# Kernel tuning notes

Hardware: AMD Instinct MI355X
Metric: run time of the kernel (lower is better)

Reference implementation:

```python
import jax, jax.numpy as jnp
import numpy as np

T, B, D = 1024, 4, 1024
E, K = 8, 2
H = int(round(2.0 * D))   # options.transformer_dim_scale = 2.0
O = D


def setup_inputs() -> dict:
    key = jax.random.key(0)
    ks = jax.random.split(key, 8)
    s = lambda fan: 1.0 / np.sqrt(fan)
    return {
        "x": jax.random.normal(ks[0], (T, B, D), dtype=jnp.float32),
        "sequence_mask": jnp.ones((T, B, 1), dtype=jnp.float32),
        "ln_scale": jnp.ones((D,), dtype=jnp.float32),
        "ln_bias": jnp.zeros((D,), dtype=jnp.float32),
        "router_w": jax.random.normal(ks[1], (E, D), dtype=jnp.float32) * s(D),
        "w1": jax.random.normal(ks[2], (E, D, H), dtype=jnp.float32) * s(D),
        "b1": jnp.zeros((E, H), dtype=jnp.float32),
        "w2": jax.random.normal(ks[3], (E, H, O), dtype=jnp.float32) * s(H),
        "b2": jnp.zeros((E, O), dtype=jnp.float32),
    }


def _layernorm(x, scale, bias, eps=1e-5):
    mu = jnp.mean(x, axis=-1, keepdims=True)
    var = jnp.mean(jnp.square(x - mu), axis=-1, keepdims=True)
    return (x - mu) * jax.lax.rsqrt(var + eps) * scale + bias


def reference(x, sequence_mask, ln_scale, ln_bias, router_w, w1, b1, w2, b2):
    t, b, d = x.shape
    n = t * b  # total tokens
    xn = _layernorm(x, ln_scale, ln_bias)
    x_flat = xn.reshape(n, d)                                  # [N, D]

    gate_logits = x_flat @ router_w.T                          # [N, E]
    topk_logits, topk_idx = jax.lax.top_k(gate_logits, K)      # [N, K]
    gate_probs = jax.nn.softmax(topk_logits, axis=-1)          # [N, K]
    # scatter top-k probs into a dense [N, E] combine-weight matrix
    rows = jnp.arange(n)[:, None]
    weights = jnp.zeros((n, E), dtype=x.dtype).at[rows, topk_idx].add(gate_probs)

    # dense per-expert two-layer MLP (exact GELU, dropout=0 at inference)
    h = jax.nn.gelu(jnp.einsum('nd,edh->neh', x_flat, w1) + b1, approximate=False)
    y = jax.nn.gelu(jnp.einsum('neh,eho->neo', h, w2) + b2, approximate=False)
    out = jnp.einsum('neo,ne->no', y, weights).reshape(t, b, O)

    out = out * sequence_mask                                  # multiplicative masking
    return out, gate_logits
```

## Files before the change

kernel.cpp:

```cpp
#include <hip/hip_runtime.h>
#include <hip/hip_bf16.h>
#include <math.h>

#define T_DIM 1024
#define B_DIM 4
#define D_DIM 1024
#define N_TOK (T_DIM * B_DIM)
#define E_NUM 8
#define K_TOP 2
#define H_DIM 2048
#define O_DIM 1024

typedef __attribute__((ext_vector_type(8))) short bf16x8;
typedef __attribute__((ext_vector_type(4))) float f32x4;

__device__ __forceinline__ float gelu_exact(float x) {
    return 0.5f * x * (1.0f + erff(x * 0.7071067811865476f));
}

__device__ __forceinline__ unsigned short f2bf(float f) {
    union { __hip_bfloat16 h; unsigned short u; } c;
    c.h = __float2bfloat16(f);
    return c.u;
}

__device__ __forceinline__ void gload_lds16(const void* g, void* l) {
    __builtin_amdgcn_global_load_lds(
        (const __attribute__((address_space(1))) void*)g,
        (__attribute__((address_space(3))) void*)l,
        16, 0, 0);
}

__global__ __launch_bounds__(256) void ln_router_kernel(
    const float* __restrict__ x,
    const float* __restrict__ seq_mask,
    const float* __restrict__ ln_scale,
    const float* __restrict__ ln_bias,
    const float* __restrict__ router_w,
    unsigned short* __restrict__ xn,
    float* __restrict__ gate_out,
    unsigned int* __restrict__ tok_e,
    float2* __restrict__ tok_p)
{
    const int wv = threadIdx.x >> 6;
    const int ln = threadIdx.x & 63;
    const int n = blockIdx.x * 4 + wv;

    const float* xr = x + (size_t)n * D_DIM;

    float v[4][4];
    float sum = 0.f, sumsq = 0.f;
#pragma unroll
    for (int p = 0; p < 4; ++p) {
        float4 t = *(const float4*)&xr[ln * 4 + p * 256];
        v[p][0] = t.x; v[p][1] = t.y; v[p][2] = t.z; v[p][3] = t.w;
#pragma unroll
        for (int c = 0; c < 4; ++c) { sum += v[p][c]; sumsq += v[p][c] * v[p][c]; }
    }
#pragma unroll
    for (int m = 1; m < 64; m <<= 1) {
        sum   += __shfl_xor(sum, m, 64);
        sumsq += __shfl_xor(sumsq, m, 64);
    }
    const float mu = sum * (1.0f / D_DIM);
    const float var = sumsq * (1.0f / D_DIM) - mu * mu;
    const float rstd = rsqrtf(var + 1e-5f);

    float xv[4][4];
#pragma unroll
    for (int p = 0; p < 4; ++p) {
        int col = ln * 4 + p * 256;
        float4 sc = *(const float4*)&ln_scale[col];
        float4 bi = *(const float4*)&ln_bias[col];
        const float* scp = (const float*)&sc;
        const float* bip = (const float*)&bi;
        ushort4 o;
        unsigned short* op = (unsigned short*)&o;
#pragma unroll
        for (int c = 0; c < 4; ++c) {
            float t = (v[p][c] - mu) * rstd * scp[c] + bip[c];
            xv[p][c] = t;
            op[c] = f2bf(t);
        }
        *(ushort4*)&xn[(size_t)n * D_DIM + col] = o;
    }

    float dot[E_NUM];
#pragma unroll
    for (int e = 0; e < E_NUM; ++e) {
        const float* rw = router_w + (size_t)e * D_DIM;
        float a = 0.f;
#pragma unroll
        for (int p = 0; p < 4; ++p) {
            float4 t = *(const float4*)&rw[ln * 4 + p * 256];
            const float* tp = (const float*)&t;
#pragma unroll
            for (int c = 0; c < 4; ++c) a += xv[p][c] * tp[c];
        }
        dot[e] = a;
    }
#pragma unroll
    for (int e = 0; e < E_NUM; ++e)
#pragma unroll
        for (int m = 1; m < 64; m <<= 1) dot[e] += __shfl_xor(dot[e], m, 64);

    if (ln == 0) {
        float4 g0 = make_float4(dot[0], dot[1], dot[2], dot[3]);
        float4 g1 = make_float4(dot[4], dot[5], dot[6], dot[7]);
        *(float4*)&gate_out[(size_t)n * E_NUM] = g0;
        *(float4*)&gate_out[(size_t)n * E_NUM + 4] = g1;

        int i0 = 0; float l0 = dot[0];
        for (int e = 1; e < E_NUM; ++e)
            if (dot[e] > l0) { l0 = dot[e]; i0 = e; }
        int i1 = -1; float l1 = -INFINITY;
        for (int e = 0; e < E_NUM; ++e) {
            if (e == i0) continue;
            if (dot[e] > l1) { l1 = dot[e]; i1 = e; }
        }
        float z = __expf(l1 - l0);
        float p0 = 1.0f / (1.0f + z);
        float p1 = z / (1.0f + z);
        float msk = seq_mask[n];

        tok_e[n] = (unsigned)i0 | ((unsigned)i1 << 8);
        tok_p[n] = make_float2(p0 * msk, p1 * msk);
    }
}

__global__ __launch_bounds__(256) void build_lists(
    const unsigned int* __restrict__ tok_e,
    const float2* __restrict__ tok_p,
    int* __restrict__ counts,
    int* __restrict__ perm,
    int* __restrict__ hrow,
    float* __restrict__ probs)
{
    const int e = blockIdx.x;
    const int tid = threadIdx.x;
    const int wv = tid >> 6, ln = tid & 63;
    __shared__ int s_base;
    __shared__ int wave_tot[4];
    if (tid == 0) s_base = 0;
    __syncthreads();

    for (int t0 = 0; t0 < N_TOK; t0 += 256) {
        int t = t0 + tid;
        unsigned pk = tok_e[t];
        int m1 = (((pk >> 8) & 0xffu) == (unsigned)e);
        int m = (((pk & 0xffu) == (unsigned)e) | m1);
        unsigned long long bal = __ballot(m);
        int pre = __popcll(bal & ((1ull << ln) - 1ull));
        if (ln == 0) wave_tot[wv] = __popcll(bal);
        __syncthreads();
        int base = s_base;
        int wbase = 0;
#pragma unroll
        for (int w = 0; w < 4; ++w) if (w < wv) wbase += wave_tot[w];
        int total = wave_tot[0] + wave_tot[1] + wave_tot[2] + wave_tot[3];
        __syncthreads();
        if (m) {
            int pos = base + wbase + pre;
            perm[e * N_TOK + pos] = t;
            hrow[e * N_TOK + pos] = t * 2 + m1;
            float2 p = tok_p[t];
            probs[e * N_TOK + pos] = m1 ? p.y : p.x;
        }
        if (tid == 0) s_base = base + total;
        __syncthreads();
    }
    if (tid == 0) counts[e] = s_base;
}

__global__ __launch_bounds__(256) void transpose_convert(
    const float* __restrict__ src, unsigned short* __restrict__ dst,
    int K, int N)
{
    __shared__ float ts[64][65];
    const int e = blockIdx.z;
    const int n0 = blockIdx.x * 64;
    const int k0 = blockIdx.y * 64;
    const float* S = src + (size_t)e * K * N;
    unsigned short* D = dst + (size_t)e * N * K;
    const int tid = threadIdx.x;
    const int r = tid >> 4, c4 = (tid & 15) * 4;

#pragma unroll
    for (int j = 0; j < 4; ++j) {
        float4 v = *(const float4*)&S[(size_t)(k0 + r + 16 * j) * N + n0 + c4];
        ts[r + 16 * j][c4 + 0] = v.x;
        ts[r + 16 * j][c4 + 1] = v.y;
        ts[r + 16 * j][c4 + 2] = v.z;
        ts[r + 16 * j][c4 + 3] = v.w;
    }
    __syncthreads();
#pragma unroll
    for (int j = 0; j < 4; ++j) {
        int nn = r + 16 * j;
        ushort4 o;
        o.x = f2bf(ts[c4 + 0][nn]);
        o.y = f2bf(ts[c4 + 1][nn]);
        o.z = f2bf(ts[c4 + 2][nn]);
        o.w = f2bf(ts[c4 + 3][nn]);
        *(ushort4*)&D[(size_t)(n0 + nn) * K + k0 + c4] = o;
    }
}

__global__ __launch_bounds__(256) void expert_gemm1(
    const unsigned short* __restrict__ xn,
    const unsigned short* __restrict__ wt1,
    const float* __restrict__ b1,
    const int* __restrict__ counts,
    const int* __restrict__ perm,
    const int* __restrict__ hrow,
    unsigned short* __restrict__ hbuf)
{
    const int e = blockIdx.z;
    const int cnt = counts[e];
    const int m0 = blockIdx.y * 128;
    if (m0 >= cnt) return;
    const int n0 = blockIdx.x * 128;
    const int tid = threadIdx.x;
    const int wv = tid >> 6, ln = tid & 63;
    const int ml = ln & 15, q = ln >> 4;
    const int wm = (wv & 1) * 64, wn = (wv >> 1) * 64;

    __shared__ __align__(16) unsigned char As[128 * 64];
    __shared__ __align__(16) unsigned char Bs[128 * 64];
    __shared__ int s_tok[128];
    __shared__ int s_hr[128];

    if (tid < 128) {
        int m = m0 + tid;
        int ok = (m < cnt);
        s_tok[tid] = ok ? perm[e * N_TOK + m] : 0;
        s_hr[tid]  = ok ? hrow[e * N_TOK + m] : 0;
    }
    __syncthreads();

    const unsigned short* wte = wt1 + (size_t)e * H_DIM * D_DIM;
    const unsigned short* agp[2]; int alds[2];
    const unsigned short* bgp[2]; int blds[2];
#pragma unroll
    for (int j = 0; j < 2; ++j) {
        int slot = j * 256 + wv * 64 + ln;
        int r = slot >> 2, ss = slot & 3;
        int sg = ss ^ ((r >> 1) & 3);
        agp[j] = xn + (size_t)s_tok[r] * D_DIM + sg * 8;
        alds[j] = slot * 16;
        bgp[j] = wte + (size_t)(n0 + r) * D_DIM + sg * 8;
        blds[j] = slot * 16;
    }

    f32x4 acc[4][4] = {};
    const int rslot = (q ^ ((ml >> 1) & 3)) * 16;

    for (int k0 = 0; k0 < D_DIM; k0 += 32) {
        __syncthreads();
#pragma unroll
        for (int j = 0; j < 2; ++j) {
            gload_lds16(agp[j] + k0, As + alds[j]);
            gload_lds16(bgp[j] + k0, Bs + blds[j]);
        }
        __syncthreads();
        bf16x8 af[4], bfr[4];
#pragma unroll
        for (int i = 0; i < 4; ++i)
            af[i] = *(const bf16x8*)(As + (wm + i * 16 + ml) * 64 + rslot);
#pragma unroll
        for (int j = 0; j < 4; ++j)
            bfr[j] = *(const bf16x8*)(Bs + (wn + j * 16 + ml) * 64 + rslot);
#pragma unroll
        for (int i = 0; i < 4; ++i)
#pragma unroll
            for (int j = 0; j < 4; ++j)
                acc[i][j] = __builtin_amdgcn_mfma_f32_16x16x32_bf16(
                    af[i], bfr[j], acc[i][j], 0, 0, 0);
    }

    float bias[4];
#pragma unroll
    for (int j = 0; j < 4; ++j)
        bias[j] = b1[(size_t)e * H_DIM + n0 + wn + j * 16 + ml];

#pragma unroll
    for (int i = 0; i < 4; ++i) {
#pragma unroll
        for (int r = 0; r < 4; ++r) {
            int rl = wm + i * 16 + q * 4 + r;
            if (m0 + rl < cnt) {
                int hr = s_hr[rl];
                unsigned short* dst = hbuf + (size_t)hr * H_DIM + n0 + wn + ml;
#pragma unroll
                for (int j = 0; j < 4; ++j)
                    dst[j * 16] = f2bf(gelu_exact(acc[i][j][r] + bias[j]));
            }
        }
    }
}

__global__ __launch_bounds__(256) void expert_gemm2(
    const unsigned short* __restrict__ hbuf,
    const unsigned short* __restrict__ wt2,
    const float* __restrict__ b2,
    const int* __restrict__ counts,
    const int* __restrict__ perm,
    const int* __restrict__ hrow,
    const float* __restrict__ probs,
    float* __restrict__ ybuf)
{
    const int e = blockIdx.z;
    const int cnt = counts[e];
    const int m0 = blockIdx.y * 128;
    if (m0 >= cnt) return;
    const int n0 = blockIdx.x * 128;
    const int tid = threadIdx.x;
    const int wv = tid >> 6, ln = tid & 63;
    const int ml = ln & 15, q = ln >> 4;
    const int wm = (wv & 1) * 64, wn = (wv >> 1) * 64;

    __shared__ __align__(16) unsigned char As[128 * 64];
    __shared__ __align__(16) unsigned char Bs[128 * 64];
    __shared__ int s_hr[128];
    __shared__ float s_p[128];

    if (tid < 128) {
        int m = m0 + tid;
        int ok = (m < cnt);
        s_hr[tid]  = ok ? hrow[e * N_TOK + m] : 0;
        s_p[tid]   = ok ? probs[e * N_TOK + m] : 0.f;
    }
    __syncthreads();

    const unsigned short* wte = wt2 + (size_t)e * O_DIM * H_DIM;
    const unsigned short* agp[2]; int alds[2];
    const unsigned short* bgp[2]; int blds[2];
#pragma unroll
    for (int j = 0; j < 2; ++j) {
        int slot = j * 256 + wv * 64 + ln;
        int r = slot >> 2, ss = slot & 3;
        int sg = ss ^ ((r >> 1) & 3);
        agp[j] = hbuf + (size_t)s_hr[r] * H_DIM + sg * 8;
        alds[j] = slot * 16;
        bgp[j] = wte + (size_t)(n0 + r) * H_DIM + sg * 8;
        blds[j] = slot * 16;
    }

    f32x4 acc[4][4] = {};
    const int rslot = (q ^ ((ml >> 1) & 3)) * 16;

    for (int k0 = 0; k0 < H_DIM; k0 += 32) {
        __syncthreads();
#pragma unroll
        for (int j = 0; j < 2; ++j) {
            gload_lds16(agp[j] + k0, As + alds[j]);
            gload_lds16(bgp[j] + k0, Bs + blds[j]);
        }
        __syncthreads();
        bf16x8 af[4], bfr[4];
#pragma unroll
        for (int i = 0; i < 4; ++i)
            af[i] = *(const bf16x8*)(As + (wm + i * 16 + ml) * 64 + rslot);
#pragma unroll
        for (int j = 0; j < 4; ++j)
            bfr[j] = *(const bf16x8*)(Bs + (wn + j * 16 + ml) * 64 + rslot);
#pragma unroll
        for (int i = 0; i < 4; ++i)
#pragma unroll
            for (int j = 0; j < 4; ++j)
                acc[i][j] = __builtin_amdgcn_mfma_f32_16x16x32_bf16(
                    af[i], bfr[j], acc[i][j], 0, 0, 0);
    }

    float bias[4];
#pragma unroll
    for (int j = 0; j < 4; ++j)
        bias[j] = b2[(size_t)e * O_DIM + n0 + wn + j * 16 + ml];

#pragma unroll
    for (int i = 0; i < 4; ++i) {
#pragma unroll
        for (int r = 0; r < 4; ++r) {
            int rl = wm + i * 16 + q * 4 + r;
            if (m0 + rl < cnt) {
                int hr = s_hr[rl];
                float p = s_p[rl];
                float* dst = ybuf + (size_t)hr * O_DIM + n0 + wn + ml;
#pragma unroll
                for (int j = 0; j < 4; ++j)
                    dst[j * 16] = gelu_exact(acc[i][j][r] + bias[j]) * p;
            }
        }
    }
}

__global__ __launch_bounds__(256) void combine_kernel(
    const float* __restrict__ ybuf, float* __restrict__ out)
{
    const size_t i = ((size_t)blockIdx.x * 256 + threadIdx.x) * 4;
    const size_t t = i / O_DIM;
    const size_t o = i % O_DIM;
    float4 a = *(const float4*)&ybuf[(t * 2) * O_DIM + o];
    float4 b = *(const float4*)&ybuf[(t * 2 + 1) * O_DIM + o];
    float4 r = make_float4(a.x + b.x, a.y + b.y, a.z + b.z, a.w + b.w);
    *(float4*)&out[i] = r;
}

extern "C" void kernel_launch(void* const* d_in, const int* in_sizes, int n_in,
                              void* d_out, int out_size, void* d_ws, size_t ws_size,
                              hipStream_t stream) {
    const float* x        = (const float*)d_in[0];
    const float* seq_mask = (const float*)d_in[1];
    const float* ln_scale = (const float*)d_in[2];
    const float* ln_bias  = (const float*)d_in[3];
    const float* router_w = (const float*)d_in[4];
    const float* w1       = (const float*)d_in[5];
    const float* b1       = (const float*)d_in[6];
    const float* w2       = (const float*)d_in[7];
    const float* b2       = (const float*)d_in[8];

    float* out      = (float*)d_out;
    float* gate_out = out + (size_t)N_TOK * O_DIM;

    char* ws = (char*)d_ws;
    unsigned short* xn = (unsigned short*)ws;
    ws += (size_t)N_TOK * D_DIM * 2;
    unsigned short* wt = (unsigned short*)ws;
    ws += (size_t)E_NUM * H_DIM * D_DIM * 2;
    unsigned short* hbuf = (unsigned short*)ws;
    ws += (size_t)N_TOK * K_TOP * H_DIM * 2;
    float* ybuf = (float*)ws;
    ws += (size_t)N_TOK * K_TOP * O_DIM * 4;
    unsigned int* tok_e = (unsigned int*)ws; ws += (size_t)N_TOK * 4;
    float2* tok_p = (float2*)ws; ws += (size_t)N_TOK * 8;
    int* counts = (int*)ws; ws += 256;
    int* perm = (int*)ws;  ws += (size_t)E_NUM * N_TOK * 4;
    int* hrow = (int*)ws;  ws += (size_t)E_NUM * N_TOK * 4;
    float* probs = (float*)ws;

    ln_router_kernel<<<N_TOK / 4, 256, 0, stream>>>(
        x, seq_mask, ln_scale, ln_bias, router_w,
        xn, gate_out, tok_e, tok_p);

    build_lists<<<E_NUM, 256, 0, stream>>>(
        tok_e, tok_p, counts, perm, hrow, probs);

    transpose_convert<<<dim3(H_DIM / 64, D_DIM / 64, E_NUM), 256, 0, stream>>>(
        w1, wt, D_DIM, H_DIM);

    expert_gemm1<<<dim3(H_DIM / 128, N_TOK / 128, E_NUM), 256, 0, stream>>>(
        xn, wt, b1, counts, perm, hrow, hbuf);

    transpose_convert<<<dim3(O_DIM / 64, H_DIM / 64, E_NUM), 256, 0, stream>>>(
        w2, wt, H_DIM, O_DIM);

    expert_gemm2<<<dim3(O_DIM / 128, N_TOK / 128, E_NUM), 256, 0, stream>>>(
        hbuf, wt, b2, counts, perm, hrow, probs, ybuf);

    combine_kernel<<<(N_TOK * O_DIM / 4) / 256, 256, 0, stream>>>(ybuf, out);
}
```

Before: 353.8 us.

## Compact expert tile grid and double K-step per LDS stage in expert GEMMs

Replaces the per-expert 3D grid, where most blocks exit early, with a flat grid of 72 slots that are mapped to (expert, row-tile) through a prefix sum over expert counts. Each main-loop iteration now loads a 64-wide K slab with a new swizzle and runs two MFMA sub-steps, which halves the number of barrier pairs. This cuts launch and scheduling waste and synchronisation overhead, at the cost of twice the LDS per block and possibly lower occupancy. The 72-slot cap assumes the total number of tiles across experts never exceeds that bound, which holds since 8192 routed rows split into at most 64+8 tiles.

```diff
diff --git a/kernel.cpp b/kernel.cpp
--- a/kernel.cpp
+++ b/kernel.cpp
@@ -10,6 +10,7 @@
 #define K_TOP 2
 #define H_DIM 2048
 #define O_DIM 1024
+#define MAX_YSLOTS 72
 
 typedef __attribute__((ext_vector_type(8))) short bf16x8;
 typedef __attribute__((ext_vector_type(4))) float f32x4;
@@ -206,6 +207,18 @@
     }
 }
 
+__device__ __forceinline__ int slot_to_tile(const int* counts, int yslot, int* m0) {
+    int e = -1, acc = 0, m = 0;
+#pragma unroll
+    for (int ee = 0; ee < E_NUM; ++ee) {
+        int t = (counts[ee] + 127) >> 7;
+        if (e < 0 && yslot < acc + t) { e = ee; m = (yslot - acc) << 7; }
+        acc += t;
+    }
+    *m0 = m;
+    return e;
+}
+
 __global__ __launch_bounds__(256) void expert_gemm1(
     const unsigned short* __restrict__ xn,
     const unsigned short* __restrict__ wt1,
@@ -215,18 +228,18 @@
     const int* __restrict__ hrow,
     unsigned short* __restrict__ hbuf)
 {
-    const int e = blockIdx.z;
+    int m0;
+    const int e = slot_to_tile(counts, blockIdx.y, &m0);
+    if (e < 0) return;
     const int cnt = counts[e];
-    const int m0 = blockIdx.y * 128;
-    if (m0 >= cnt) return;
     const int n0 = blockIdx.x * 128;
     const int tid = threadIdx.x;
     const int wv = tid >> 6, ln = tid & 63;
     const int ml = ln & 15, q = ln >> 4;
     const int wm = (wv & 1) * 64, wn = (wv >> 1) * 64;
 
-    __shared__ __align__(16) unsigned char As[128 * 64];
-    __shared__ __align__(16) unsigned char Bs[128 * 64];
+    __shared__ __align__(16) unsigned char As[128 * 128];
+    __shared__ __align__(16) unsigned char Bs[128 * 128];
     __shared__ int s_tok[128];
     __shared__ int s_hr[128];
 
@@ -239,13 +252,13 @@
     __syncthreads();
 
     const unsigned short* wte = wt1 + (size_t)e * H_DIM * D_DIM;
-    const unsigned short* agp[2]; int alds[2];
-    const unsigned short* bgp[2]; int blds[2];
-#pragma unroll
-    for (int j = 0; j < 2; ++j) {
-        int slot = j * 256 + wv * 64 + ln;
-        int r = slot >> 2, ss = slot & 3;
-        int sg = ss ^ ((r >> 1) & 3);
+    const unsigned short* agp[4]; int alds[4];
+    const unsigned short* bgp[4]; int blds[4];
+#pragma unroll
+    for (int j = 0; j < 4; ++j) {
+        int slot = j * 256 + tid;
+        int r = slot >> 3, c = slot & 7;
+        int sg = (c & 4) | ((c & 3) ^ ((r >> 1) & 3));
         agp[j] = xn + (size_t)s_tok[r] * D_DIM + sg * 8;
         alds[j] = slot * 16;
         bgp[j] = wte + (size_t)(n0 + r) * D_DIM + sg * 8;
@@ -255,27 +268,30 @@
     f32x4 acc[4][4] = {};
     const int rslot = (q ^ ((ml >> 1) & 3)) * 16;
 
-    for (int k0 = 0; k0 < D_DIM; k0 += 32) {
-        __syncthreads();
-#pragma unroll
-        for (int j = 0; j < 2; ++j) {
+    for (int k0 = 0; k0 < D_DIM; k0 += 64) {
+        __syncthreads();
+#pragma unroll
+        for (int j = 0; j < 4; ++j) {
             gload_lds16(agp[j] + k0, As + alds[j]);
             gload_lds16(bgp[j] + k0, Bs + blds[j]);
         }
         __syncthreads();
-        bf16x8 af[4], bfr[4];
-#pragma unroll
-        for (int i = 0; i < 4; ++i)
-            af[i] = *(const bf16x8*)(As + (wm + i * 16 + ml) * 64 + rslot);
-#pragma unroll
-        for (int j = 0; j < 4; ++j)
-            bfr[j] = *(const bf16x8*)(Bs + (wn + j * 16 + ml) * 64 + rslot);
-#pragma unroll
-        for (int i = 0; i < 4; ++i)
+#pragma unroll
+        for (int t = 0; t < 2; ++t) {
+            bf16x8 af[4], bfr[4];
+#pragma unroll
+            for (int i = 0; i < 4; ++i)
+                af[i] = *(const bf16x8*)(As + (wm + i * 16 + ml) * 128 + t * 64 + rslot);
 #pragma unroll
             for (int j = 0; j < 4; ++j)
-                acc[i][j] = __builtin_amdgcn_mfma_f32_16x16x32_bf16(
-                    af[i], bfr[j], acc[i][j], 0, 0, 0);
+                bfr[j] = *(const bf16x8*)(Bs + (wn + j * 16 + ml) * 128 + t * 64 + rslot);
+#pragma unroll
+            for (int i = 0; i < 4; ++i)
+#pragma unroll
+                for (int j = 0; j < 4; ++j)
+                    acc[i][j] = __builtin_amdgcn_mfma_f32_16x16x32_bf16(
+                        af[i], bfr[j], acc[i][j], 0, 0, 0);
+        }
     }
 
     float bias[4];
@@ -309,18 +325,18 @@
     const float* __restrict__ probs,
     float* __restrict__ ybuf)
 {
-    const int e = blockIdx.z;
+    int m0;
+    const int e = slot_to_tile(counts, blockIdx.y, &m0);
+    if (e < 0) return;
     const int cnt = counts[e];
-    const int m0 = blockIdx.y * 128;
-    if (m0 >= cnt) return;
     const int n0 = blockIdx.x * 128;
     const int tid = threadIdx.x;
     const int wv = tid >> 6, ln = tid & 63;
     const int ml = ln & 15, q = ln >> 4;
     const int wm = (wv & 1) * 64, wn = (wv >> 1) * 64;
 
-    __shared__ __align__(16) unsigned char As[128 * 64];
-    __shared__ __align__(16) unsigned char Bs[128 * 64];
+    __shared__ __align__(16) unsigned char As[128 * 128];
+    __shared__ __align__(16) unsigned char Bs[128 * 128];
     __shared__ int s_hr[128];
     __shared__ float s_p[128];
 
@@ -333,13 +349,13 @@
     __syncthreads();
 
     const unsigned short* wte = wt2 + (size_t)e * O_DIM * H_DIM;
-    const unsigned short* agp[2]; int alds[2];
-    const unsigned short* bgp[2]; int blds[2];
-#pragma unroll
-    for (int j = 0; j < 2; ++j) {
-        int slot = j * 256 + wv * 64 + ln;
-        int r = slot >> 2, ss = slot & 3;
-        int sg = ss ^ ((r >> 1) & 3);
+    const unsigned short* agp[4]; int alds[4];
+    const unsigned short* bgp[4]; int blds[4];
+#pragma unroll
+    for (int j = 0; j < 4; ++j) {
+        int slot = j * 256 + tid;
+        int r = slot >> 3, c = slot & 7;
+        int sg = (c & 4) | ((c & 3) ^ ((r >> 1) & 3));
         agp[j] = hbuf + (size_t)s_hr[r] * H_DIM + sg * 8;
         alds[j] = slot * 16;
         bgp[j] = wte + (size_t)(n0 + r) * H_DIM + sg * 8;
@@ -349,27 +365,30 @@
     f32x4 acc[4][4] = {};
     const int rslot = (q ^ ((ml >> 1) & 3)) * 16;
 
-    for (int k0 = 0; k0 < H_DIM; k0 += 32) {
-        __syncthreads();
-#pragma unroll
-        for (int j = 0; j < 2; ++j) {
+    for (int k0 = 0; k0 < H_DIM; k0 += 64) {
+        __syncthreads();
+#pragma unroll
+        for (int j = 0; j < 4; ++j) {
             gload_lds16(agp[j] + k0, As + alds[j]);
             gload_lds16(bgp[j] + k0, Bs + blds[j]);
         }
         __syncthreads();
-        bf16x8 af[4], bfr[4];
-#pragma unroll
-        for (int i = 0; i < 4; ++i)
-            af[i] = *(const bf16x8*)(As + (wm + i * 16 + ml) * 64 + rslot);
-#pragma unroll
-        for (int j = 0; j < 4; ++j)
-            bfr[j] = *(const bf16x8*)(Bs + (wn + j * 16 + ml) * 64 + rslot);
-#pragma unroll
-        for (int i = 0; i < 4; ++i)
+#pragma unroll
+        for (int t = 0; t < 2; ++t) {
+            bf16x8 af[4], bfr[4];
+#pragma unroll
+            for (int i = 0; i < 4; ++i)
+                af[i] = *(const bf16x8*)(As + (wm + i * 16 + ml) * 128 + t * 64 + rslot);
 #pragma unroll
             for (int j = 0; j < 4; ++j)
-                acc[i][j] = __builtin_amdgcn_mfma_f32_16x16x32_bf16(
-                    af[i], bfr[j], acc[i][j], 0, 0, 0);
+                bfr[j] = *(const bf16x8*)(Bs + (wn + j * 16 + ml) * 128 + t * 64 + rslot);
+#pragma unroll
+            for (int i = 0; i < 4; ++i)
+#pragma unroll
+                for (int j = 0; j < 4; ++j)
+                    acc[i][j] = __builtin_amdgcn_mfma_f32_16x16x32_bf16(
+                        af[i], bfr[j], acc[i][j], 0, 0, 0);
+        }
     }
 
     float bias[4];
@@ -448,13 +467,13 @@
     transpose_convert<<<dim3(H_DIM / 64, D_DIM / 64, E_NUM), 256, 0, stream>>>(
         w1, wt, D_DIM, H_DIM);
 
-    expert_gemm1<<<dim3(H_DIM / 128, N_TOK / 128, E_NUM), 256, 0, stream>>>(
+    expert_gemm1<<<dim3(H_DIM / 128, MAX_YSLOTS), 256, 0, stream>>>(
         xn, wt, b1, counts, perm, hrow, hbuf);
 
     transpose_convert<<<dim3(O_DIM / 64, H_DIM / 64, E_NUM), 256, 0, stream>>>(
         w2, wt, H_DIM, O_DIM);
 
-    expert_gemm2<<<dim3(O_DIM / 128, N_TOK / 128, E_NUM), 256, 0, stream>>>(
+    expert_gemm2<<<dim3(O_DIM / 128, MAX_YSLOTS), 256, 0, stream>>>(
         hbuf, wt, b2, counts, perm, hrow, probs, ybuf);
 
     combine_kernel<<<(N_TOK * O_DIM / 4) / 256, 256, 0, stream>>>(ybuf, out);
```

Result: slower. 374.5 us (+5.9%).

## Compact expert tile grid and use 512-thread blocks for second expert GEMM

Applied to the files above, without the earlier changes.

Replaces the per-expert z-dimension grid, where most blocks exit early, with a compact list of M-tile slots mapped to experts by a prefix sum over per-expert counts. Both expert GEMMs launch a fixed 72 slots, which covers the worst case of 8192 routed rows plus padding of at most one partial tile per expert. The second GEMM now runs 8 waves per block with 32x64 warp tiles and one async load per thread, aiming for more latency hiding. In exchange every block recomputes the slot mapping and the second GEMM does less register-level reuse per wave.

```diff
diff --git a/kernel.cpp b/kernel.cpp
--- a/kernel.cpp
+++ b/kernel.cpp
@@ -10,6 +10,7 @@
 #define K_TOP 2
 #define H_DIM 2048
 #define O_DIM 1024
+#define MAX_YSLOTS 72
 
 typedef __attribute__((ext_vector_type(8))) short bf16x8;
 typedef __attribute__((ext_vector_type(4))) float f32x4;
@@ -206,6 +207,18 @@
     }
 }
 
+__device__ __forceinline__ int slot_to_tile(const int* counts, int yslot, int* m0) {
+    int e = -1, acc = 0, m = 0;
+#pragma unroll
+    for (int ee = 0; ee < E_NUM; ++ee) {
+        int t = (counts[ee] + 127) >> 7;
+        if (e < 0 && yslot < acc + t) { e = ee; m = (yslot - acc) << 7; }
+        acc += t;
+    }
+    *m0 = m;
+    return e;
+}
+
 __global__ __launch_bounds__(256) void expert_gemm1(
     const unsigned short* __restrict__ xn,
     const unsigned short* __restrict__ wt1,
@@ -215,10 +228,10 @@
     const int* __restrict__ hrow,
     unsigned short* __restrict__ hbuf)
 {
-    const int e = blockIdx.z;
+    int m0;
+    const int e = slot_to_tile(counts, blockIdx.y, &m0);
+    if (e < 0) return;
     const int cnt = counts[e];
-    const int m0 = blockIdx.y * 128;
-    if (m0 >= cnt) return;
     const int n0 = blockIdx.x * 128;
     const int tid = threadIdx.x;
     const int wv = tid >> 6, ln = tid & 63;
@@ -243,7 +256,7 @@
     const unsigned short* bgp[2]; int blds[2];
 #pragma unroll
     for (int j = 0; j < 2; ++j) {
-        int slot = j * 256 + wv * 64 + ln;
+        int slot = j * 256 + tid;
         int r = slot >> 2, ss = slot & 3;
         int sg = ss ^ ((r >> 1) & 3);
         agp[j] = xn + (size_t)s_tok[r] * D_DIM + sg * 8;
@@ -299,7 +312,7 @@
     }
 }
 
-__global__ __launch_bounds__(256) void expert_gemm2(
+__global__ __launch_bounds__(512) void expert_gemm2(
     const unsigned short* __restrict__ hbuf,
     const unsigned short* __restrict__ wt2,
     const float* __restrict__ b2,
@@ -309,15 +322,16 @@
     const float* __restrict__ probs,
     float* __restrict__ ybuf)
 {
-    const int e = blockIdx.z;
+    int m0;
+    const int e = slot_to_tile(counts, blockIdx.y, &m0);
+    if (e < 0) return;
     const int cnt = counts[e];
-    const int m0 = blockIdx.y * 128;
-    if (m0 >= cnt) return;
     const int n0 = blockIdx.x * 128;
     const int tid = threadIdx.x;
     const int wv = tid >> 6, ln = tid & 63;
     const int ml = ln & 15, q = ln >> 4;
-    const int wm = (wv & 1) * 64, wn = (wv >> 1) * 64;
+    const int wm = (wv & 3) * 32;
+    const int wn = (wv >> 2) * 64;
 
     __shared__ __align__(16) unsigned char As[128 * 64];
     __shared__ __align__(16) unsigned char Bs[128 * 64];
@@ -327,45 +341,36 @@
     if (tid < 128) {
         int m = m0 + tid;
         int ok = (m < cnt);
-        s_hr[tid]  = ok ? hrow[e * N_TOK + m] : 0;
-        s_p[tid]   = ok ? probs[e * N_TOK + m] : 0.f;
+        s_hr[tid] = ok ? hrow[e * N_TOK + m] : 0;
+        s_p[tid]  = ok ? probs[e * N_TOK + m] : 0.f;
     }
     __syncthreads();
 
     const unsigned short* wte = wt2 + (size_t)e * O_DIM * H_DIM;
-    const unsigned short* agp[2]; int alds[2];
-    const unsigned short* bgp[2]; int blds[2];
-#pragma unroll
-    for (int j = 0; j < 2; ++j) {
-        int slot = j * 256 + wv * 64 + ln;
-        int r = slot >> 2, ss = slot & 3;
-        int sg = ss ^ ((r >> 1) & 3);
-        agp[j] = hbuf + (size_t)s_hr[r] * H_DIM + sg * 8;
-        alds[j] = slot * 16;
-        bgp[j] = wte + (size_t)(n0 + r) * H_DIM + sg * 8;
-        blds[j] = slot * 16;
-    }
-
-    f32x4 acc[4][4] = {};
+    const int r_ = tid >> 2, ss = tid & 3;
+    const int sg = ss ^ ((r_ >> 1) & 3);
+    const unsigned short* agp = hbuf + (size_t)s_hr[r_] * H_DIM + sg * 8;
+    const int alds = tid * 16;
+    const unsigned short* bgp = wte + (size_t)(n0 + r_) * H_DIM + sg * 8;
+    const int blds = tid * 16;
+
+    f32x4 acc[2][4] = {};
     const int rslot = (q ^ ((ml >> 1) & 3)) * 16;
 
     for (int k0 = 0; k0 < H_DIM; k0 += 32) {
         __syncthreads();
-#pragma unroll
-        for (int j = 0; j < 2; ++j) {
-            gload_lds16(agp[j] + k0, As + alds[j]);
-            gload_lds16(bgp[j] + k0, Bs + blds[j]);
-        }
-        __syncthreads();
-        bf16x8 af[4], bfr[4];
-#pragma unroll
-        for (int i = 0; i < 4; ++i)
+        gload_lds16(agp + k0, As + alds);
+        gload_lds16(bgp + k0, Bs + blds);
+        __syncthreads();
+        bf16x8 af[2], bfr[4];
+#pragma unroll
+        for (int i = 0; i < 2; ++i)
             af[i] = *(const bf16x8*)(As + (wm + i * 16 + ml) * 64 + rslot);
 #pragma unroll
         for (int j = 0; j < 4; ++j)
             bfr[j] = *(const bf16x8*)(Bs + (wn + j * 16 + ml) * 64 + rslot);
 #pragma unroll
-        for (int i = 0; i < 4; ++i)
+        for (int i = 0; i < 2; ++i)
 #pragma unroll
             for (int j = 0; j < 4; ++j)
                 acc[i][j] = __builtin_amdgcn_mfma_f32_16x16x32_bf16(
@@ -378,7 +383,7 @@
         bias[j] = b2[(size_t)e * O_DIM + n0 + wn + j * 16 + ml];
 
 #pragma unroll
-    for (int i = 0; i < 4; ++i) {
+    for (int i = 0; i < 2; ++i) {
 #pragma unroll
         for (int r = 0; r < 4; ++r) {
             int rl = wm + i * 16 + q * 4 + r;
@@ -448,13 +453,13 @@
     transpose_convert<<<dim3(H_DIM / 64, D_DIM / 64, E_NUM), 256, 0, stream>>>(
         w1, wt, D_DIM, H_DIM);
 
-    expert_gemm1<<<dim3(H_DIM / 128, N_TOK / 128, E_NUM), 256, 0, stream>>>(
+    expert_gemm1<<<dim3(H_DIM / 128, MAX_YSLOTS), 256, 0, stream>>>(
         xn, wt, b1, counts, perm, hrow, hbuf);
 
     transpose_convert<<<dim3(O_DIM / 64, H_DIM / 64, E_NUM), 256, 0, stream>>>(
         w2, wt, H_DIM, O_DIM);
 
-    expert_gemm2<<<dim3(O_DIM / 128, N_TOK / 128, E_NUM), 256, 0, stream>>>(
+    expert_gemm2<<<dim3(O_DIM / 128, MAX_YSLOTS), 512, 0, stream>>>(
         hbuf, wt, b2, counts, perm, hrow, probs, ybuf);
 
     combine_kernel<<<(N_TOK * O_DIM / 4) / 256, 256, 0, stream>>>(ybuf, out);
```

New measurement: 348.6 us. About the same (-1.5%).
